# Kernel optimization log

Measured on AMD Instinct MI355X. Metric: run time of the kernel, lower is better.

Reference implementation:

```python
import jax, jax.numpy as jnp
import numpy as np

# Per-task block sizes, sorted descending (powers of 2), as in _InverseLogDetCache
N = (262144, 65536, 16384)
TOTAL = 262144 + 65536 + 16384  # 344064
DIAG_SHIFT = 10.0  # keeps Schur complement S away from 0 (plays role of noise)


def setup_inputs() -> dict:
    key = jax.random.key(0)
    ks = jax.random.split(key, 14)
    rn = lambda k, n: jax.random.normal(k, (n,), dtype=jnp.float32)
    return {
        "lam00_re": rn(ks[0], N[0]) + DIAG_SHIFT,
        "lam00_im": rn(ks[1], N[0]),
        "lam01_re": rn(ks[2], N[0]),
        "lam01_im": rn(ks[3], N[0]),
        "lam02_re": rn(ks[4], N[0]),
        "lam02_im": rn(ks[5], N[0]),
        "lam11_re": rn(ks[6], N[1]) + DIAG_SHIFT,
        "lam11_im": rn(ks[7], N[1]),
        "lam12_re": rn(ks[8], N[1]),
        "lam12_im": rn(ks[9], N[1]),
        "lam22_re": rn(ks[10], N[2]) + DIAG_SHIFT,
        "lam22_im": rn(ks[11], N[2]),
        "z_re": rn(ks[12], TOTAL),
        "z_im": rn(ks[13], TOTAL),
    }


def _step(A, B, lam_ll, n_l):
    """One recursive block Schur-complement update.
    A: (Ra, Ra, na) complex current inverse; B: (Ra*r, n_l) off-diag lam block;
    lam_ll: (n_l,) diagonal lam; returns updated A (R+1, R+1, n_l) and logdet inc."""
    Ra, na = A.shape[0], A.shape[-1]
    r = na // n_l
    Bvec = B.reshape(Ra, -1)                              # (Ra, na)
    T = (Bvec[None, :, :] * A).sum(1).reshape(-1, n_l)    # (R, n_l), R = Ra*r
    M = (B.conj() * T).sum(0)                             # (n_l,)
    S = lam_ll - M                                        # Schur complement diag
    logdet_inc = jnp.log(jnp.abs(S)).sum()
    P = T / S                                             # (R, n_l)
    C = P[:, None, :] * T[None, :, :].conj()              # (R, R, n_l)
    # scatter-add old inverse A into the refined block structure of C
    ii0, ii1, ii2 = jnp.meshgrid(jnp.arange(Ra), jnp.arange(Ra), jnp.arange(na), indexing='ij')
    ii0, ii1, ii2 = ii0.ravel(), ii1.ravel(), ii2.ravel()
    jj0 = ii2 % n_l
    jj1 = ii2 // n_l
    C = C.at[ii0 * r + jj1, ii1 * r + jj1, jj0].add(A.reshape(-1))
    ur = jnp.concatenate([C, -P[:, None, :]], axis=1)                       # (R, R+1, n_l)
    br = jnp.concatenate([-P.conj()[None, :, :], (1.0 / S)[None, None, :]], axis=1)  # (1, R+1, n_l)
    return jnp.concatenate([ur, br], axis=0), logdet_inc


def _forward(lams, z):
    A = (1.0 / lams[(0, 0)])[None, None, :]               # (1, 1, N[0])
    logdet = jnp.log(jnp.abs(lams[(0, 0)])).sum()
    for l in range(1, len(N)):
        B = jnp.concatenate([lams[(k, l)] for k in range(l)], axis=0).reshape(-1, N[l])
        A, inc = _step(A, B, lams[(l, l)], N[l])
        logdet = logdet + inc
    # tilde-to-tilde gram matrix solve: z (TOTAL,) -> (1, R, n_min) * A, sum block rows
    n_min = N[-1]
    zb = z.reshape(1, -1, n_min)                          # (1, 21, n_min)
    zout = (zb * A).sum(-2).reshape(-1)                   # (TOTAL,)
    return A, logdet, zout


def reference(lam00_re, lam00_im, lam01_re, lam01_im, lam02_re, lam02_im,
              lam11_re, lam11_im, lam12_re, lam12_im, lam22_re, lam22_im,
              z_re, z_im):
    lams = {
        (0, 0): lam00_re + 1j * lam00_im,
        (0, 1): lam01_re + 1j * lam01_im,
        (0, 2): lam02_re + 1j * lam02_im,
        (1, 1): lam11_re + 1j * lam11_im,
        (1, 2): lam12_re + 1j * lam12_im,
        (2, 2): lam22_re + 1j * lam22_im,
    }
    z = z_re + 1j * z_im
    A, logdet, zout = _forward(lams, z)
    return (jnp.stack([A.real, A.imag]), logdet, jnp.stack([zout.real, zout.imag]))
```

## Files before the change

### kernel.cpp

```cpp
#include <hip/hip_runtime.h>

#define N2 16384
#define N1 65536

#define OUT_AIM 7225344
#define OUT_LD  14450688
#define OUT_ZRE 14450689
#define OUT_ZIM 14794753

#define L_T2R  0
#define L_T2I  1280
#define L_M2   2560
#define L_SC   3072
#define L_IS2R 9728
#define L_IS2I 9792
#define L_RED  9856
#define L_TOT  9864

#define SC(idx, u, jl) lds[L_SC + (((idx)*4 + (u)) * 64) + (jl)]

#define NTST2(addr, v0, v1) do {                                   \
    union { float f[2]; long L; } _u; _u.f[0] = (v0); _u.f[1] = (v1); \
    __builtin_nontemporal_store(_u.L, (long*)(addr)); } while (0)

__global__ __launch_bounds__(448) void fused_kernel(
    const float* __restrict__ l00r, const float* __restrict__ l00i,
    const float* __restrict__ l01r, const float* __restrict__ l01i,
    const float* __restrict__ l02r, const float* __restrict__ l02i,
    const float* __restrict__ l11r, const float* __restrict__ l11i,
    const float* __restrict__ l12r, const float* __restrict__ l12i,
    const float* __restrict__ l22r, const float* __restrict__ l22i,
    const float* __restrict__ zre,  const float* __restrict__ zim,
    float* __restrict__ out)
{
    __shared__ float lds[L_TOT];
    const int t   = threadIdx.x;
    const int jl  = t & 63;
    const int j0  = blockIdx.x * 64;
    const bool y0 = (blockIdx.y == 0);
    float ld = 0.f;

    if (t < 256) {
        const int u = t >> 6;
        const int m = u * N2 + (j0 + jl);

        float i0r[4], i0i[4], t1r[4], t1i[4], p1r[4], p1i[4];
        float m1r = 0.f, m1i = 0.f;
#pragma unroll
        for (int k = 0; k < 4; ++k) {
            const int i = k * N1 + m;
            const float ar = l00r[i], ai = l00i[i];
            const float br = l01r[i], bi = l01i[i];
            const float d  = ar*ar + ai*ai;
            const float rd = 1.f / d;
            if (y0) ld += 0.5f * logf(d);
            const float xr = ar * rd, xi = -ai * rd;
            i0r[k] = xr; i0i[k] = xi;
            const float tr = br*xr - bi*xi;
            const float ti = br*xi + bi*xr;
            t1r[k] = tr; t1i[k] = ti;
            m1r += br*tr + bi*ti;
            m1i += br*ti - bi*tr;
        }
        const float s1r = l11r[m] - m1r;
        const float s1i = l11i[m] - m1i;
        const float ds1 = s1r*s1r + s1i*s1i;
        if (y0) ld += 0.5f * logf(ds1);
        const float rds1 = 1.f / ds1;
        const float is1r = s1r * rds1, is1i = -s1i * rds1;
#pragma unroll
        for (int k = 0; k < 4; ++k) {
            p1r[k] = t1r[k]*is1r - t1i[k]*is1i;
            p1i[k] = t1r[k]*is1i + t1i[k]*is1r;
        }

        float bcr[5], bci[5];
#pragma unroll
        for (int a = 0; a < 4; ++a) { bcr[a] = l02r[a*N1+m]; bci[a] = l02i[a*N1+m]; }
        bcr[4] = l12r[m]; bci[4] = l12i[m];

        float wr = -bcr[4], wi = -bci[4];
#pragma unroll
        for (int b = 0; b < 4; ++b) {
            wr += bcr[b]*t1r[b] + bci[b]*t1i[b];
            wi += bci[b]*t1r[b] - bcr[b]*t1i[b];
        }
        float ur[5], ui[5];
#pragma unroll
        for (int a = 0; a < 4; ++a) {
            ur[a] = p1r[a]*wr - p1i[a]*wi + bcr[a]*i0r[a] - bci[a]*i0i[a];
            ui[a] = p1r[a]*wi + p1i[a]*wr + bcr[a]*i0i[a] + bci[a]*i0r[a];
        }
        {
            float vr = bcr[4]*is1r - bci[4]*is1i;
            float vi = bcr[4]*is1i + bci[4]*is1r;
#pragma unroll
            for (int b = 0; b < 4; ++b) {
                vr -= bcr[b]*p1r[b] + bci[b]*p1i[b];
                vi -= bci[b]*p1r[b] - bcr[b]*p1i[b];
            }
            ur[4] = vr; ui[4] = vi;
        }
        float m2r = 0.f, m2i = 0.f;
#pragma unroll
        for (int a = 0; a < 5; ++a) {
            lds[L_T2R + (a*4+u)*64 + jl] = ur[a];
            lds[L_T2I + (a*4+u)*64 + jl] = ui[a];
            m2r += bcr[a]*ur[a] + bci[a]*ui[a];
            m2i += bcr[a]*ui[a] - bci[a]*ur[a];
        }
        lds[L_M2 + (0*4+u)*64 + jl] = m2r;
        lds[L_M2 + (1*4+u)*64 + jl] = m2i;
#pragma unroll
        for (int b = 0; b < 4; ++b) {
            SC(b,      u, jl) = t1r[b];  SC(4+b,  u, jl) = t1i[b];
            SC(8+b,    u, jl) = p1r[b];  SC(12+b, u, jl) = p1i[b];
            SC(16+b,   u, jl) = i0r[b];  SC(20+b, u, jl) = i0i[b];
        }
        SC(24, u, jl) = is1r;  SC(25, u, jl) = is1i;
    }
    __syncthreads();

    if (t < 64) {
        float s2r = l22r[j0 + t], s2i = l22i[j0 + t];
#pragma unroll
        for (int u = 0; u < 4; ++u) {
            s2r -= lds[L_M2 + (0*4+u)*64 + t];
            s2i -= lds[L_M2 + (1*4+u)*64 + t];
        }
        const float ds2  = s2r*s2r + s2i*s2i;
        const float rds2 = 1.f / ds2;
        lds[L_IS2R + t] =  s2r * rds2;
        lds[L_IS2I + t] = -s2i * rds2;
        if (y0) ld += 0.5f * logf(ds2);
    }
    __syncthreads();

    const int g  = t >> 6;
    const int p  = blockIdx.y * 7 + g;
    const int l  = t & 63;
    const int h  = l >> 5;
    const int c  = l & 31;
    const int c2 = 2*c;
    const int j2 = j0 + c2;

    const float is2r0 = lds[L_IS2R + c2],   is2r1 = lds[L_IS2R + c2+1];
    const float is2i0 = lds[L_IS2I + c2],   is2i1 = lds[L_IS2I + c2+1];

    float zar0=0.f, zai0=0.f, zar1=0.f, zai1=0.f;

    if (p == 20) {
#pragma unroll
        for (int qi = 0; qi < 11; ++qi) {
            const int q = 2*qi + h;
            if (q >= 21) continue;
            float ar0, ai0, ar1, ai1;
            if (q < 20) {
                const float tr0 = lds[L_T2R + q*64 + c2], tr1 = lds[L_T2R + q*64 + c2+1];
                const float ti0 = lds[L_T2I + q*64 + c2], ti1 = lds[L_T2I + q*64 + c2+1];
                ar0 = -(tr0*is2r0 - ti0*is2i0);  ai0 = tr0*is2i0 + ti0*is2r0;
                ar1 = -(tr1*is2r1 - ti1*is2i1);  ai1 = tr1*is2i1 + ti1*is2r1;
            } else { ar0=is2r0; ai0=is2i0; ar1=is2r1; ai1=is2i1; }
            NTST2(out + (p*21+q)*N2 + j2,           ar0, ar1);
            NTST2(out + OUT_AIM + (p*21+q)*N2 + j2, ai0, ai1);
            const float zr0 = zre[q*N2+j2], zr1 = zre[q*N2+j2+1];
            const float zi0 = zim[q*N2+j2], zi1 = zim[q*N2+j2+1];
            zar0 += zr0*ar0 - zi0*ai0;  zai0 += zr0*ai0 + zi0*ar0;
            zar1 += zr1*ar1 - zi1*ai1;  zai1 += zr1*ai1 + zi1*ar1;
        }
    } else {
        const int a_p = p >> 2, u_p = p & 3;
        const float tpr0 = lds[L_T2R + p*64 + c2], tpr1 = lds[L_T2R + p*64 + c2+1];
        const float tpi0 = lds[L_T2I + p*64 + c2], tpi1 = lds[L_T2I + p*64 + c2+1];
        const float ppr0 = tpr0*is2r0 - tpi0*is2i0, ppi0 = tpr0*is2i0 + tpi0*is2r0;
        const float ppr1 = tpr1*is2r1 - tpi1*is2i1, ppi1 = tpr1*is2i1 + tpi1*is2r1;
        float par0=0.f, pai0=0.f, par1=0.f, pai1=0.f;
        if (a_p < 4) {
            par0 = SC(8+a_p,  u_p, c2);   pai0 = SC(12+a_p, u_p, c2);
            par1 = SC(8+a_p,  u_p, c2+1); pai1 = SC(12+a_p, u_p, c2+1);
        }
#pragma unroll
        for (int qi = 0; qi < 11; ++qi) {
            const int q = 2*qi + h;
            if (q >= 21) continue;
            float ar0, ai0, ar1, ai1;
            if (q < 20) {
                const float tr0 = lds[L_T2R + q*64 + c2], tr1 = lds[L_T2R + q*64 + c2+1];
                const float ti0 = lds[L_T2I + q*64 + c2], ti1 = lds[L_T2I + q*64 + c2+1];
                ar0 = ppr0*tr0 + ppi0*ti0;  ai0 = ppi0*tr0 - ppr0*ti0;
                ar1 = ppr1*tr1 + ppi1*ti1;  ai1 = ppi1*tr1 - ppr1*ti1;
                if ((q & 3) == u_p) {
                    const int b = q >> 2;
                    if (a_p < 4) {
                        if (b < 4) {
                            const float tbr0 = SC(b, u_p, c2),   tbi0 = SC(4+b, u_p, c2);
                            const float tbr1 = SC(b, u_p, c2+1), tbi1 = SC(4+b, u_p, c2+1);
                            ar0 += par0*tbr0 + pai0*tbi0;  ai0 += pai0*tbr0 - par0*tbi0;
                            ar1 += par1*tbr1 + pai1*tbi1;  ai1 += pai1*tbr1 - par1*tbi1;
                            if (b == a_p) {
                                ar0 += SC(16+a_p, u_p, c2);   ai0 += SC(20+a_p, u_p, c2);
                                ar1 += SC(16+a_p, u_p, c2+1); ai1 += SC(20+a_p, u_p, c2+1);
                            }
                        } else { ar0 -= par0; ai0 -= pai0; ar1 -= par1; ai1 -= pai1; }
                    } else {
                        if (b < 4) {
                            ar0 -= SC(8+b, u_p, c2);   ai0 += SC(12+b, u_p, c2);
                            ar1 -= SC(8+b, u_p, c2+1); ai1 += SC(12+b, u_p, c2+1);
                        } else {
                            ar0 += SC(24, u_p, c2);   ai0 += SC(25, u_p, c2);
                            ar1 += SC(24, u_p, c2+1); ai1 += SC(25, u_p, c2+1);
                        }
                    }
                }
            } else { ar0 = -ppr0; ai0 = -ppi0; ar1 = -ppr1; ai1 = -ppi1; }
            NTST2(out + (p*21+q)*N2 + j2,           ar0, ar1);
            NTST2(out + OUT_AIM + (p*21+q)*N2 + j2, ai0, ai1);
            const float zr0 = zre[q*N2+j2], zr1 = zre[q*N2+j2+1];
            const float zi0 = zim[q*N2+j2], zi1 = zim[q*N2+j2+1];
            zar0 += zr0*ar0 - zi0*ai0;  zai0 += zr0*ai0 + zi0*ar0;
            zar1 += zr1*ar1 - zi1*ai1;  zai1 += zr1*ai1 + zi1*ar1;
        }
    }

    zar0 += __shfl_xor(zar0, 32, 64);  zai0 += __shfl_xor(zai0, 32, 64);
    zar1 += __shfl_xor(zar1, 32, 64);  zai1 += __shfl_xor(zai1, 32, 64);
    {
        const int src = l >> 1;
        const float e_r = __shfl(zar0, src, 64), o_r = __shfl(zar1, src, 64);
        const float e_i = __shfl(zai0, src, 64), o_i = __shfl(zai1, src, 64);
        const float zvr = (l & 1) ? o_r : e_r;
        const float zvi = (l & 1) ? o_i : e_i;
        if (p != 0 || blockIdx.x >= 8)
            __builtin_nontemporal_store(zvr, out + OUT_ZRE + p*N2 + j0 + l);
        __builtin_nontemporal_store(zvi, out + OUT_ZIM + p*N2 + j0 + l);
    }

    if (y0) {
        float v = ld;
#pragma unroll
        for (int off = 32; off > 0; off >>= 1) v += __shfl_down(v, off, 64);
        __syncthreads();
        if (jl == 0) lds[L_RED + g] = v;
        __syncthreads();
        if (t == 0) {
            double s = 0.0;
#pragma unroll
            for (int w = 0; w < 7; ++w) s += (double)lds[L_RED + w];
            out[OUT_ZRE + 2*blockIdx.x]     = __int_as_float(__double2hiint(s));
            out[OUT_ZRE + 2*blockIdx.x + 1] = __int_as_float(__double2loint(s));
        }
    }
}

__global__ __launch_bounds__(512) void finalize_kernel(
    const float* __restrict__ zre, const float* __restrict__ zim,
    float* __restrict__ out)
{
    const int t = threadIdx.x;
    double v = 0.0;
    if (t < 256) {
        const int hi = __float_as_int(out[OUT_ZRE + 2*t]);
        const int lo = __float_as_int(out[OUT_ZRE + 2*t + 1]);
        v = __hiloint2double(hi, lo);
    }
#pragma unroll
    for (int off = 32; off > 0; off >>= 1) v += __shfl_down(v, off, 64);
    __shared__ double wsum[8];
    if ((t & 63) == 0) wsum[t >> 6] = v;
    __syncthreads();

    float acc = 0.f;
#pragma unroll
    for (int q = 0; q < 21; ++q) {
        const float ar = out[q*N2 + t];
        const float ai = out[OUT_AIM + q*N2 + t];
        acc = fmaf(zre[q*N2 + t],  ar, acc);
        acc = fmaf(-zim[q*N2 + t], ai, acc);
    }
    out[OUT_ZRE + t] = acc;

    if (t == 0) {
        double s = 0.0;
#pragma unroll
        for (int w = 0; w < 8; ++w) s += wsum[w];
        out[OUT_LD] = (float)s;
    }
}

extern "C" void kernel_launch(void* const* d_in, const int* in_sizes, int n_in,
                              void* d_out, int out_size, void* d_ws, size_t ws_size,
                              hipStream_t stream)
{
    (void)d_ws; (void)ws_size;
    const float* l00r = (const float*)d_in[0];
    const float* l00i = (const float*)d_in[1];
    const float* l01r = (const float*)d_in[2];
    const float* l01i = (const float*)d_in[3];
    const float* l02r = (const float*)d_in[4];
    const float* l02i = (const float*)d_in[5];
    const float* l11r = (const float*)d_in[6];
    const float* l11i = (const float*)d_in[7];
    const float* l12r = (const float*)d_in[8];
    const float* l12i = (const float*)d_in[9];
    const float* l22r = (const float*)d_in[10];
    const float* l22i = (const float*)d_in[11];
    const float* zre  = (const float*)d_in[12];
    const float* zim  = (const float*)d_in[13];
    float* out        = (float*)d_out;

    fused_kernel<<<dim3(N2/64, 3), dim3(448), 0, stream>>>(
        l00r,l00i,l01r,l01i,l02r,l02i,l11r,l11i,l12r,l12i,l22r,l22i,
        zre,zim, out);
    finalize_kernel<<<1, 512, 0, stream>>>(zre, zim, out);
}
```

Measured before the change: 113.9 us.

## Merge three y-blocks into one so each block handles three output rows

The grid drops from 3 y-blocks to 1, and each wave now computes three output row slots (p = g, g+7, g+14) inside one loop over q. The shared LDS T2 values and z loads are reused across the three slots. This removes the prologue (loading lam arrays and Schur complements) that was recomputed in every y-block. The cost is 256 blocks instead of 768 and more registers per thread, which may lower occupancy and latency hiding for a store-bound kernel.

```diff
diff --git a/kernel.cpp b/kernel.cpp
--- a/kernel.cpp
+++ b/kernel.cpp
@@ -22,6 +22,78 @@
 #define NTST2(addr, v0, v1) do {                                   \
     union { float f[2]; long L; } _u; _u.f[0] = (v0); _u.f[1] = (v1); \
     __builtin_nontemporal_store(_u.L, (long*)(addr)); } while (0)
+
+#define SLOT_PREP(s, P)                                                       \
+    const int  p##s    = (P);                                                 \
+    const bool is20_##s = (p##s == 20);                                       \
+    const int  ap_##s  = p##s >> 2, up_##s = p##s & 3;                        \
+    float ppr0_##s=0.f, ppi0_##s=0.f, ppr1_##s=0.f, ppi1_##s=0.f;             \
+    float par0_##s=0.f, pai0_##s=0.f, par1_##s=0.f, pai1_##s=0.f;             \
+    if (!is20_##s) {                                                          \
+        const float tpr0 = lds[L_T2R + p##s*64 + c2], tpr1 = lds[L_T2R + p##s*64 + c2+1]; \
+        const float tpi0 = lds[L_T2I + p##s*64 + c2], tpi1 = lds[L_T2I + p##s*64 + c2+1]; \
+        ppr0_##s = tpr0*is2r0 - tpi0*is2i0;  ppi0_##s = tpr0*is2i0 + tpi0*is2r0; \
+        ppr1_##s = tpr1*is2r1 - tpi1*is2i1;  ppi1_##s = tpr1*is2i1 + tpi1*is2r1; \
+        if (ap_##s < 4) {                                                     \
+            par0_##s = SC(8+ap_##s,  up_##s, c2);   pai0_##s = SC(12+ap_##s, up_##s, c2);   \
+            par1_##s = SC(8+ap_##s,  up_##s, c2+1); pai1_##s = SC(12+ap_##s, up_##s, c2+1); \
+        }                                                                     \
+    }                                                                         \
+    float zar0_##s=0.f, zai0_##s=0.f, zar1_##s=0.f, zai1_##s=0.f;
+
+#define SLOT_Q(s) do {                                                        \
+    float ar0, ai0, ar1, ai1;                                                 \
+    if (is20_##s) {                                                           \
+        if (q < 20) {                                                         \
+            ar0 = -(tr0*is2r0 - ti0*is2i0);  ai0 = tr0*is2i0 + ti0*is2r0;     \
+            ar1 = -(tr1*is2r1 - ti1*is2i1);  ai1 = tr1*is2i1 + ti1*is2r1;     \
+        } else { ar0=is2r0; ai0=is2i0; ar1=is2r1; ai1=is2i1; }                \
+    } else if (q < 20) {                                                      \
+        ar0 = ppr0_##s*tr0 + ppi0_##s*ti0;  ai0 = ppi0_##s*tr0 - ppr0_##s*ti0;\
+        ar1 = ppr1_##s*tr1 + ppi1_##s*ti1;  ai1 = ppi1_##s*tr1 - ppr1_##s*ti1;\
+        if ((q & 3) == up_##s) {                  \
+            const int b = q >> 2;                                             \
+            if (ap_##s < 4) {                                                 \
+                if (b < 4) {                                                  \
+                    const float tbr0 = SC(b, up_##s, c2),   tbi0 = SC(4+b, up_##s, c2);   \
+                    const float tbr1 = SC(b, up_##s, c2+1), tbi1 = SC(4+b, up_##s, c2+1); \
+                    ar0 += par0_##s*tbr0 + pai0_##s*tbi0;  ai0 += pai0_##s*tbr0 - par0_##s*tbi0; \
+                    ar1 += par1_##s*tbr1 + pai1_##s*tbi1;  ai1 += pai1_##s*tbr1 - par1_##s*tbi1; \
+                    if (b == ap_##s) {                         \
+                        ar0 += SC(16+ap_##s, up_##s, c2);   ai0 += SC(20+ap_##s, up_##s, c2);   \
+                        ar1 += SC(16+ap_##s, up_##s, c2+1); ai1 += SC(20+ap_##s, up_##s, c2+1); \
+                    }                                                         \
+                } else { ar0 -= par0_##s; ai0 -= pai0_##s; ar1 -= par1_##s; ai1 -= pai1_##s; } \
+            } else {                                                          \
+                if (b < 4) {                                \
+                    ar0 -= SC(8+b, up_##s, c2);   ai0 += SC(12+b, up_##s, c2);   \
+                    ar1 -= SC(8+b, up_##s, c2+1); ai1 += SC(12+b, up_##s, c2+1); \
+                } else {                                            \
+                    ar0 += SC(24, up_##s, c2);   ai0 += SC(25, up_##s, c2);   \
+                    ar1 += SC(24, up_##s, c2+1); ai1 += SC(25, up_##s, c2+1); \
+                }                                                             \
+            }                                                                 \
+        }                                                                     \
+    } else { ar0 = -ppr0_##s; ai0 = -ppi0_##s; ar1 = -ppr1_##s; ai1 = -ppi1_##s; } \
+    NTST2(out + (p##s*21+q)*N2 + j2,           ar0, ar1);                     \
+    NTST2(out + OUT_AIM + (p##s*21+q)*N2 + j2, ai0, ai1);                     \
+    zar0_##s += zr0*ar0 - zi0*ai0;  zai0_##s += zr0*ai0 + zi0*ar0;            \
+    zar1_##s += zr1*ar1 - zi1*ai1;  zai1_##s += zr1*ai1 + zi1*ar1;            \
+} while (0)
+
+#define SLOT_ZSTORE(s) do {                                                   \
+    float a0 = zar0_##s, b0 = zai0_##s, a1 = zar1_##s, b1 = zai1_##s;         \
+    a0 += __shfl_xor(a0, 32, 64);  b0 += __shfl_xor(b0, 32, 64);              \
+    a1 += __shfl_xor(a1, 32, 64);  b1 += __shfl_xor(b1, 32, 64);              \
+    const int src = l >> 1;                                                   \
+    const float e_r = __shfl(a0, src, 64), o_r = __shfl(a1, src, 64);         \
+    const float e_i = __shfl(b0, src, 64), o_i = __shfl(b1, src, 64);         \
+    const float zvr = (l & 1) ? o_r : e_r;                                    \
+    const float zvi = (l & 1) ? o_i : e_i;                                    \
+    if (p##s != 0 || blockIdx.x >= 8)              \
+        __builtin_nontemporal_store(zvr, out + OUT_ZRE + p##s*N2 + j0 + l);   \
+    __builtin_nontemporal_store(zvi, out + OUT_ZIM + p##s*N2 + j0 + l);       \
+} while (0)
 
 __global__ __launch_bounds__(448) void fused_kernel(
     const float* __restrict__ l00r, const float* __restrict__ l00i,
@@ -37,7 +109,6 @@
     const int t   = threadIdx.x;
     const int jl  = t & 63;
     const int j0  = blockIdx.x * 64;
-    const bool y0 = (blockIdx.y == 0);
     float ld = 0.f;
 
     if (t < 256) {
@@ -53,7 +124,7 @@
             const float br = l01r[i], bi = l01i[i];
             const float d  = ar*ar + ai*ai;
             const float rd = 1.f / d;
-            if (y0) ld += 0.5f * logf(d);
+            ld += 0.5f * logf(d);
             const float xr = ar * rd, xi = -ai * rd;
             i0r[k] = xr; i0i[k] = xi;
             const float tr = br*xr - bi*xi;
@@ -65,7 +136,7 @@
         const float s1r = l11r[m] - m1r;
         const float s1i = l11i[m] - m1i;
         const float ds1 = s1r*s1r + s1i*s1i;
-        if (y0) ld += 0.5f * logf(ds1);
+        ld += 0.5f * logf(ds1);
         const float rds1 = 1.f / ds1;
         const float is1r = s1r * rds1, is1i = -s1i * rds1;
 #pragma unroll
@@ -132,12 +203,11 @@
         const float rds2 = 1.f / ds2;
         lds[L_IS2R + t] =  s2r * rds2;
         lds[L_IS2I + t] = -s2i * rds2;
-        if (y0) ld += 0.5f * logf(ds2);
+        ld += 0.5f * logf(ds2);
     }
     __syncthreads();
 
     const int g  = t >> 6;
-    const int p  = blockIdx.y * 7 + g;
     const int l  = t & 63;
     const int h  = l >> 5;
     const int c  = l & 31;
@@ -147,95 +217,31 @@
     const float is2r0 = lds[L_IS2R + c2],   is2r1 = lds[L_IS2R + c2+1];
     const float is2i0 = lds[L_IS2I + c2],   is2i1 = lds[L_IS2I + c2+1];
 
-    float zar0=0.f, zai0=0.f, zar1=0.f, zai1=0.f;
-
-    if (p == 20) {
-#pragma unroll
-        for (int qi = 0; qi < 11; ++qi) {
-            const int q = 2*qi + h;
-            if (q >= 21) continue;
-            float ar0, ai0, ar1, ai1;
-            if (q < 20) {
-                const float tr0 = lds[L_T2R + q*64 + c2], tr1 = lds[L_T2R + q*64 + c2+1];
-                const float ti0 = lds[L_T2I + q*64 + c2], ti1 = lds[L_T2I + q*64 + c2+1];
-                ar0 = -(tr0*is2r0 - ti0*is2i0);  ai0 = tr0*is2i0 + ti0*is2r0;
-                ar1 = -(tr1*is2r1 - ti1*is2i1);  ai1 = tr1*is2i1 + ti1*is2r1;
-            } else { ar0=is2r0; ai0=is2i0; ar1=is2r1; ai1=is2i1; }
-            NTST2(out + (p*21+q)*N2 + j2,           ar0, ar1);
-            NTST2(out + OUT_AIM + (p*21+q)*N2 + j2, ai0, ai1);
-            const float zr0 = zre[q*N2+j2], zr1 = zre[q*N2+j2+1];
-            const float zi0 = zim[q*N2+j2], zi1 = zim[q*N2+j2+1];
-            zar0 += zr0*ar0 - zi0*ai0;  zai0 += zr0*ai0 + zi0*ar0;
-            zar1 += zr1*ar1 - zi1*ai1;  zai1 += zr1*ai1 + zi1*ar1;
-        }
-    } else {
-        const int a_p = p >> 2, u_p = p & 3;
-        const float tpr0 = lds[L_T2R + p*64 + c2], tpr1 = lds[L_T2R + p*64 + c2+1];
-        const float tpi0 = lds[L_T2I + p*64 + c2], tpi1 = lds[L_T2I + p*64 + c2+1];
-        const float ppr0 = tpr0*is2r0 - tpi0*is2i0, ppi0 = tpr0*is2i0 + tpi0*is2r0;
-        const float ppr1 = tpr1*is2r1 - tpi1*is2i1, ppi1 = tpr1*is2i1 + tpi1*is2r1;
-        float par0=0.f, pai0=0.f, par1=0.f, pai1=0.f;
-        if (a_p < 4) {
-            par0 = SC(8+a_p,  u_p, c2);   pai0 = SC(12+a_p, u_p, c2);
-            par1 = SC(8+a_p,  u_p, c2+1); pai1 = SC(12+a_p, u_p, c2+1);
-        }
-#pragma unroll
-        for (int qi = 0; qi < 11; ++qi) {
-            const int q = 2*qi + h;
-            if (q >= 21) continue;
-            float ar0, ai0, ar1, ai1;
-            if (q < 20) {
-                const float tr0 = lds[L_T2R + q*64 + c2], tr1 = lds[L_T2R + q*64 + c2+1];
-                const float ti0 = lds[L_T2I + q*64 + c2], ti1 = lds[L_T2I + q*64 + c2+1];
-                ar0 = ppr0*tr0 + ppi0*ti0;  ai0 = ppi0*tr0 - ppr0*ti0;
-                ar1 = ppr1*tr1 + ppi1*ti1;  ai1 = ppi1*tr1 - ppr1*ti1;
-                if ((q & 3) == u_p) {
-                    const int b = q >> 2;
-                    if (a_p < 4) {
-                        if (b < 4) {
-                            const float tbr0 = SC(b, u_p, c2),   tbi0 = SC(4+b, u_p, c2);
-                            const float tbr1 = SC(b, u_p, c2+1), tbi1 = SC(4+b, u_p, c2+1);
-                            ar0 += par0*tbr0 + pai0*tbi0;  ai0 += pai0*tbr0 - par0*tbi0;
-                            ar1 += par1*tbr1 + pai1*tbi1;  ai1 += pai1*tbr1 - par1*tbi1;
-                            if (b == a_p) {
-                                ar0 += SC(16+a_p, u_p, c2);   ai0 += SC(20+a_p, u_p, c2);
-                                ar1 += SC(16+a_p, u_p, c2+1); ai1 += SC(20+a_p, u_p, c2+1);
-                            }
-                        } else { ar0 -= par0; ai0 -= pai0; ar1 -= par1; ai1 -= pai1; }
-                    } else {
-                        if (b < 4) {
-                            ar0 -= SC(8+b, u_p, c2);   ai0 += SC(12+b, u_p, c2);
-                            ar1 -= SC(8+b, u_p, c2+1); ai1 += SC(12+b, u_p, c2+1);
-                        } else {
-                            ar0 += SC(24, u_p, c2);   ai0 += SC(25, u_p, c2);
-                            ar1 += SC(24, u_p, c2+1); ai1 += SC(25, u_p, c2+1);
-                        }
-                    }
-                }
-            } else { ar0 = -ppr0; ai0 = -ppi0; ar1 = -ppr1; ai1 = -ppi1; }
-            NTST2(out + (p*21+q)*N2 + j2,           ar0, ar1);
-            NTST2(out + OUT_AIM + (p*21+q)*N2 + j2, ai0, ai1);
-            const float zr0 = zre[q*N2+j2], zr1 = zre[q*N2+j2+1];
-            const float zi0 = zim[q*N2+j2], zi1 = zim[q*N2+j2+1];
-            zar0 += zr0*ar0 - zi0*ai0;  zai0 += zr0*ai0 + zi0*ar0;
-            zar1 += zr1*ar1 - zi1*ai1;  zai1 += zr1*ai1 + zi1*ar1;
-        }
-    }
-
-    zar0 += __shfl_xor(zar0, 32, 64);  zai0 += __shfl_xor(zai0, 32, 64);
-    zar1 += __shfl_xor(zar1, 32, 64);  zai1 += __shfl_xor(zai1, 32, 64);
+    SLOT_PREP(0, g)
+    SLOT_PREP(1, g + 7)
+    SLOT_PREP(2, g + 14)
+
+#pragma unroll
+    for (int qi = 0; qi < 11; ++qi) {
+        const int q = 2*qi + h;
+        if (q >= 21) continue;
+        float tr0=0.f, tr1=0.f, ti0=0.f, ti1=0.f;
+        if (q < 20) {
+            tr0 = lds[L_T2R + q*64 + c2];  tr1 = lds[L_T2R + q*64 + c2+1];
+            ti0 = lds[L_T2I + q*64 + c2];  ti1 = lds[L_T2I + q*64 + c2+1];
+        }
+        const float zr0 = zre[q*N2+j2], zr1 = zre[q*N2+j2+1];
+        const float zi0 = zim[q*N2+j2], zi1 = zim[q*N2+j2+1];
+        SLOT_Q(0);
+        SLOT_Q(1);
+        SLOT_Q(2);
+    }
+
+    SLOT_ZSTORE(0);
+    SLOT_ZSTORE(1);
+    SLOT_ZSTORE(2);
+
     {
-        const int src = l >> 1;
-        const float e_r = __shfl(zar0, src, 64), o_r = __shfl(zar1, src, 64);
-        const float e_i = __shfl(zai0, src, 64), o_i = __shfl(zai1, src, 64);
-        const float zvr = (l & 1) ? o_r : e_r;
-        const float zvi = (l & 1) ? o_i : e_i;
-        if (p != 0 || blockIdx.x >= 8)
-            __builtin_nontemporal_store(zvr, out + OUT_ZRE + p*N2 + j0 + l);
-        __builtin_nontemporal_store(zvi, out + OUT_ZIM + p*N2 + j0 + l);
-    }
-
-    if (y0) {
         float v = ld;
 #pragma unroll
         for (int off = 32; off > 0; off >>= 1) v += __shfl_down(v, off, 64);
@@ -308,7 +314,7 @@
     const float* zim  = (const float*)d_in[13];
     float* out        = (float*)d_out;
 
-    fused_kernel<<<dim3(N2/64, 3), dim3(448), 0, stream>>>(
+    fused_kernel<<<dim3(N2/64, 1), dim3(448), 0, stream>>>(
         l00r,l00i,l01r,l01i,l02r,l02i,l11r,l11i,l12r,l12i,l22r,l22i,
         zre,zim, out);
     finalize_kernel<<<1, 512, 0, stream>>>(zre, zim, out);
```

New measurement: 112.3 us. No clear change (-1.4%).
